# Performance work log

Hardware: AMD Instinct MI355X
Metric: run time of the kernel (lower is better)

## Reference

```python
import jax, jax.numpy as jnp
import numpy as np


def log_g(x):
    # Appendix B.3 of 'Were RNNs All We Needed?'
    return jnp.where(x >= 0, jnp.log(jax.nn.relu(x) + 0.5), -jax.nn.softplus(-x))


def parallel_scan_log(log_a, log_b):
    # h[0] = b[0]; h[i] = a[i]*h[i-1] + b[i], computed in log space along axis 1
    log_a_star = jnp.cumsum(log_a, axis=1)
    log_x0_plus_b_star = jax.lax.cumlogsumexp(log_b - log_a_star, axis=1)
    return jnp.exp(log_a_star + log_x0_plus_b_star)


def setup_inputs() -> dict:
    key = jax.random.key(0)
    B, T, D = 8, 4096, 1024
    k1, k2, k3, k4, k5 = jax.random.split(key, 5)
    scale = 1.0 / np.sqrt(D)
    return {
        "h_prev_layer": jax.random.normal(k1, (B, T, D), dtype=jnp.float32),
        "W_z": jax.random.uniform(k2, (D, D), jnp.float32, -scale, scale),
        "b_z": jax.random.uniform(k3, (D,), jnp.float32, -scale, scale),
        "W_h": jax.random.uniform(k4, (D, D), jnp.float32, -scale, scale),
        "b_h": jax.random.uniform(k5, (D,), jnp.float32, -scale, scale),
    }


def reference(h_prev_layer, W_z, b_z, W_h, b_h):
    k = jnp.einsum('btd,ed->bte', h_prev_layer, W_z) + b_z          # linear_z
    tilde_h = jnp.einsum('btd,ed->bte', h_prev_layer, W_h) + b_h    # linear_h
    log_z = -jax.nn.softplus(-k)
    log_one_minus_z = -jax.nn.softplus(k)
    log_tilde_h = log_g(tilde_h)
    return parallel_scan_log(log_one_minus_z, log_z + log_tilde_h)
```

## Files before the change

kernel.cpp:

```cpp
#include <hip/hip_runtime.h>
#include <hip/hip_fp16.h>

typedef float f32x4 __attribute__((ext_vector_type(4)));
typedef __bf16 bf16x8 __attribute__((ext_vector_type(8)));

#define BB_ 8
#define TT_ 4096
#define DD_ 1024
#define MM_ (BB_*TT_)
#define KK_ DD_

#define NCH 64
#define LCH (TT_/NCH)

static __device__ __forceinline__ unsigned short f2bf_rn(float f) {
  unsigned int u = __float_as_uint(f);
  u += 0x7FFFu + ((u >> 16) & 1u);
  return (unsigned short)(u >> 16);
}

__global__ void cvt_f32_bf16(const float4* __restrict__ src,
                             ushort4* __restrict__ dst, int n4) {
  int stride = gridDim.x * blockDim.x;
  for (int i = blockIdx.x * blockDim.x + threadIdx.x; i < n4; i += stride) {
    float4 v = src[i];
    ushort4 o;
    o.x = f2bf_rn(v.x); o.y = f2bf_rn(v.y);
    o.z = f2bf_rn(v.z); o.w = f2bf_rn(v.w);
    dst[i] = o;
  }
}

__device__ __forceinline__ void gload_lds16(const void* g, void* l) {
  __builtin_amdgcn_global_load_lds(
      (const __attribute__((address_space(1))) void*)g,
      (__attribute__((address_space(3))) void*)l, 16, 0, 0);
}

#define STA(q, nb_, kkh) gload_lds16(pXa + (q) * 65536 + (kkh), (nb_) + (q) * 8192 + wofs)
#define STB(q, nb_, kkh) gload_lds16(pWb + (q) * 65536 + (kkh), (nb_) + 32768 + (q) * 8192 + wofs)

#define PHASE(cb_, mh, kh, STAGEOPS, WAITOPS) do {                          \
    const char* Ab_ = (cb_);                                                \
    const char* Bb_ = (cb_) + 32768;                                        \
    const int sk_ = (kh) ? sk1 : sk0;                                       \
    bf16x8 af_[4];                                                          \
    _Pragma("unroll")                                                       \
    for (int ii = 0; ii < 4; ++ii)                                          \
      af_[ii] = *reinterpret_cast<const bf16x8*>(                           \
          Ab_ + rA7 + (mh) * 8192 + ii * 2048 + sk_);                       \
    if ((mh) == 0) {                                                        \
      _Pragma("unroll")                                                     \
      for (int j = 0; j < 4; ++j)                                           \
        bfv[j] = *reinterpret_cast<const bf16x8*>(                          \
            Bb_ + rB7 + j * 2048 + sk_);                                    \
    }                                                                       \
    STAGEOPS;                                                               \
    WAITOPS;                                                                \
    __builtin_amdgcn_s_barrier();                                           \
    asm volatile("s_waitcnt lgkmcnt(0)" ::: "memory");                      \
    __builtin_amdgcn_sched_barrier(0);                                      \
    __builtin_amdgcn_s_setprio(1);                                          \
    _Pragma("unroll")                                                       \
    for (int ii = 0; ii < 4; ++ii)                                          \
      _Pragma("unroll")                                                     \
      for (int j = 0; j < 4; ++j)                                           \
        acc[(mh) * 4 + ii][j] = __builtin_amdgcn_mfma_f32_16x16x32_bf16(    \
            af_[ii], bfv[j], acc[(mh) * 4 + ii][j], 0, 0, 0);               \
    __builtin_amdgcn_s_setprio(0);                                          \
    asm volatile("" ::: "memory");                                          \
    __builtin_amdgcn_s_barrier();                                           \
  } while (0)

__global__ __launch_bounds__(512, 2) void gemm_fused(
    const unsigned short* __restrict__ Xb,
    const unsigned short* __restrict__ Wb,
    const float* __restrict__ bz, const float* __restrict__ bh,
    __half* __restrict__ Zb, __half* __restrict__ Gb)
{
  extern __shared__ __align__(16) char smem[];
  const int tid  = threadIdx.x;
  const int wave = tid >> 6;
  const int lane = tid & 63;
  const int wm = wave >> 2, wn = wave & 3;
  const int fr = lane & 15, kg = lane >> 4, fx = fr & 7;

  int swz = (blockIdx.x & 7) * 128 + (blockIdx.x >> 3);
  const int m0 = (swz >> 3) * 256;
  const int e0 = (swz & 7) * 256;

  const int arow = tid >> 3;
  const int aslx = ((tid & 7) ^ (arow & 7)) * 8;
  const unsigned short* pXa = Xb + (size_t)(m0 + arow) * KK_ + aslx;
  const unsigned short* pWb = Wb + (size_t)(e0 + arow) * KK_ + aslx;
  const int wofs = wave * 1024;

  const int rA7 = (wm * 128 + fr) * 128;
  const int rB7 = (wn * 64 + fr) * 128;
  const int sk0 = (kg ^ fx) * 16;
  const int sk1 = sk0 ^ 64;

  f32x4 acc[8][4];
  #pragma unroll
  for (int i = 0; i < 8; i++)
    #pragma unroll
    for (int j = 0; j < 4; j++)
      acc[i][j] = (f32x4){0.f, 0.f, 0.f, 0.f};
  bf16x8 bfv[4];

  STA(0, smem, 0); STA(2, smem, 0); STB(0, smem, 0);
  STB(1, smem, 0); STB(2, smem, 0); STB(3, smem, 0);
  STA(1, smem, 0); STA(3, smem, 0);
  asm volatile("s_waitcnt vmcnt(2)" ::: "memory");
  __builtin_amdgcn_s_barrier();

  #pragma unroll 1
  for (int t = 0; t < 15; ++t) {
    char* cb = smem + ((t & 1) << 16);
    char* nb = smem + (((t + 1) & 1) << 16);
    const int kn = (t + 1) * 64;
    PHASE(cb, 0, 0, {STA(0, nb, kn); STA(2, nb, kn); STB(0, nb, kn);},
          asm volatile("s_waitcnt vmcnt(3)" ::: "memory"));
    PHASE(cb, 1, 0, {STB(1, nb, kn); STB(2, nb, kn); STB(3, nb, kn);}, );
    PHASE(cb, 0, 1, {STA(1, nb, kn); STA(3, nb, kn);}, );
    PHASE(cb, 1, 1, {},
          asm volatile("s_waitcnt vmcnt(2)" ::: "memory"));
  }
  {
    char* cb = smem + 65536;
    PHASE(cb, 0, 0, {}, asm volatile("s_waitcnt vmcnt(0)" ::: "memory"));
    PHASE(cb, 1, 0, {}, );
    PHASE(cb, 0, 1, {}, );
    PHASE(cb, 1, 1, {}, );
  }

  const bool isZ = (e0 < DD_);
  const float* bias = isZ ? bz : bh;
  __half* outp = isZ ? Zb : Gb;
  const int ec0 = (isZ ? e0 : (e0 - DD_)) + wn * 64;

  float bv[4];
  #pragma unroll
  for (int j = 0; j < 4; j++) bv[j] = bias[ec0 + j * 16 + fr];

  __half* ew = (__half*)(smem + wave * 9216);
  const int sub = lane & 7, rowr = lane >> 3;

  #pragma unroll
  for (int p = 0; p < 2; ++p) {
    #pragma unroll
    for (int ii = 0; ii < 4; ++ii) {
      #pragma unroll
      for (int j = 0; j < 4; ++j) {
        #pragma unroll
        for (int r = 0; r < 4; ++r) {
          float val = acc[p * 4 + ii][j][r] + bv[j];
          float res;
          if (isZ) {
            res = 1.0f / (1.0f + __expf(-val));
          } else {
            res = (val >= 0.0f) ? (val + 0.5f)
                                : (1.0f / (1.0f + __expf(-val)));
          }
          ew[(ii * 16 + kg * 4 + r) * 72 + j * 16 + fr] = __float2half(res);
        }
      }
    }
    #pragma unroll
    for (int q = 0; q < 8; ++q) {
      int rl = q * 8 + rowr;
      uint4 v = *reinterpret_cast<const uint4*>(&ew[rl * 72 + sub * 8]);
      size_t rg = (size_t)(m0 + wm * 128 + p * 64 + rl);
      *reinterpret_cast<uint4*>(&outp[rg * DD_ + ec0 + sub * 8]) = v;
    }
  }
}

__global__ __launch_bounds__(256) void scan_partial(
    const ushort4* __restrict__ Z, const ushort4* __restrict__ G,
    float4* __restrict__ P, float4* __restrict__ Q) {
  const int d4 = threadIdx.x;
  const int c  = blockIdx.x;
  const int b  = blockIdx.y;
  size_t base = ((size_t)b * TT_ + (size_t)c * LCH) * (DD_ / 4) + d4;
  float p0=1.f,p1=1.f,p2=1.f,p3=1.f, q0=0.f,q1=0.f,q2=0.f,q3=0.f;
  for (int t = 0; t < LCH; ++t) {
    ushort4 uz = Z[base + (size_t)t * (DD_ / 4)];
    ushort4 ug = G[base + (size_t)t * (DD_ / 4)];
    float z, g, a;
    z = __half2float(__ushort_as_half(uz.x)); g = __half2float(__ushort_as_half(ug.x));
    a = 1.f - z; p0 *= a; q0 = fmaf(a, q0, z * g);
    z = __half2float(__ushort_as_half(uz.y)); g = __half2float(__ushort_as_half(ug.y));
    a = 1.f - z; p1 *= a; q1 = fmaf(a, q1, z * g);
    z = __half2float(__ushort_as_half(uz.z)); g = __half2float(__ushort_as_half(ug.z));
    a = 1.f - z; p2 *= a; q2 = fmaf(a, q2, z * g);
    z = __half2float(__ushort_as_half(uz.w)); g = __half2float(__ushort_as_half(ug.w));
    a = 1.f - z; p3 *= a; q3 = fmaf(a, q3, z * g);
  }
  size_t o = ((size_t)b * NCH + c) * (DD_ / 4) + d4;
  P[o] = make_float4(p0, p1, p2, p3);
  Q[o] = make_float4(q0, q1, q2, q3);
}

__global__ __launch_bounds__(256) void scan_combine(
    const float4* __restrict__ P, const float4* __restrict__ Q,
    float4* __restrict__ H) {
  const int d4 = threadIdx.x;
  const int b  = blockIdx.x;
  float4 h = make_float4(0.f, 0.f, 0.f, 0.f);
  for (int c = 0; c < NCH; ++c) {
    size_t o = ((size_t)b * NCH + c) * (DD_ / 4) + d4;
    H[o] = h;
    float4 p = P[o], q = Q[o];
    h.x = fmaf(p.x, h.x, q.x);
    h.y = fmaf(p.y, h.y, q.y);
    h.z = fmaf(p.z, h.z, q.z);
    h.w = fmaf(p.w, h.w, q.w);
  }
}

__global__ __launch_bounds__(256) void scan_apply(
    const ushort4* __restrict__ Z, const ushort4* __restrict__ G,
    const float4* __restrict__ H, float4* __restrict__ out) {
  const int d4 = threadIdx.x;
  const int c  = blockIdx.x;
  const int b  = blockIdx.y;
  float4 h = H[((size_t)b * NCH + c) * (DD_ / 4) + d4];
  size_t base = ((size_t)b * TT_ + (size_t)c * LCH) * (DD_ / 4) + d4;
  for (int t = 0; t < LCH; ++t) {
    ushort4 uz = Z[base + (size_t)t * (DD_ / 4)];
    ushort4 ug = G[base + (size_t)t * (DD_ / 4)];
    float z, g, a;
    z = __half2float(__ushort_as_half(uz.x)); g = __half2float(__ushort_as_half(ug.x));
    a = 1.f - z; h.x = fmaf(a, h.x, z * g);
    z = __half2float(__ushort_as_half(uz.y)); g = __half2float(__ushort_as_half(ug.y));
    a = 1.f - z; h.y = fmaf(a, h.y, z * g);
    z = __half2float(__ushort_as_half(uz.z)); g = __half2float(__ushort_as_half(ug.z));
    a = 1.f - z; h.z = fmaf(a, h.z, z * g);
    z = __half2float(__ushort_as_half(uz.w)); g = __half2float(__ushort_as_half(ug.w));
    a = 1.f - z; h.w = fmaf(a, h.w, z * g);
    out[base + (size_t)t * (DD_ / 4)] = h;
  }
}

extern "C" void kernel_launch(void* const* d_in, const int* in_sizes, int n_in,
                              void* d_out, int out_size, void* d_ws, size_t ws_size,
                              hipStream_t stream) {
  const float* X  = (const float*)d_in[0];
  const float* Wz = (const float*)d_in[1];
  const float* bz = (const float*)d_in[2];
  const float* Wh = (const float*)d_in[3];
  const float* bh = (const float*)d_in[4];
  float* out = (float*)d_out;

  const size_t szXb = (size_t)MM_ * DD_ * 2;
  const size_t szWb = (size_t)2 * DD_ * DD_ * 2;
  const size_t szZ  = (size_t)MM_ * DD_ * 2;
  const size_t szPQ = (size_t)BB_ * NCH * DD_ * 4;

  char* ws = (char*)d_ws;
  unsigned short *Xb, *Wb;
  __half *Zb, *Gb;
  const size_t needA = szXb + szWb + 2 * szZ + 3 * szPQ;
  if (ws_size >= needA) {
    Xb = (unsigned short*)ws;              ws += szXb;
    Wb = (unsigned short*)ws;              ws += szWb;
  } else {
    Xb = (unsigned short*)d_out;
    Wb = (unsigned short*)((char*)d_out + szXb);
  }
  Zb = (__half*)ws;  ws += szZ;
  Gb = (__half*)ws;  ws += szZ;
  float* P = (float*)ws;  ws += szPQ;
  float* Q = (float*)ws;  ws += szPQ;
  float* H = (float*)ws;

  cvt_f32_bf16<<<2048, 256, 0, stream>>>((const float4*)X, (ushort4*)Xb,
                                         (int)((size_t)MM_ * DD_ / 4));
  cvt_f32_bf16<<<512, 256, 0, stream>>>((const float4*)Wz, (ushort4*)Wb,
                                        DD_ * DD_ / 4);
  cvt_f32_bf16<<<512, 256, 0, stream>>>((const float4*)Wh,
                                        (ushort4*)(Wb + (size_t)DD_ * DD_),
                                        DD_ * DD_ / 4);
  gemm_fused<<<(MM_ / 256) * ((2 * DD_) / 256), 512, 131072, stream>>>(
      Xb, Wb, bz, bh, Zb, Gb);

  scan_partial<<<dim3(NCH, BB_), 256, 0, stream>>>((const ushort4*)Zb, (const ushort4*)Gb,
                                                   (float4*)P, (float4*)Q);
  scan_combine<<<BB_, 256, 0, stream>>>((const float4*)P, (const float4*)Q, (float4*)H);
  scan_apply<<<dim3(NCH, BB_), 256, 0, stream>>>((const ushort4*)Zb, (const ushort4*)Gb,
                                                 (const float4*)H, (float4*)out);
}
```

Baseline: 280.1 us.

## Double-buffer LDS fragment registers to overlap ds_reads with MFMA in GEMM mainloop

Restructures the GEMM main loop so the LDS fragment reads for the next phase go into a second register set while the current phase's MFMAs execute. Partial lgkmcnt waits (8) replace full drains. All eight global-to-LDS stages for the next tile are now issued together, with a single vmcnt(0) wait before that buffer is consumed. This aims to hide LDS read latency behind matrix math, at the cost of more VGPRs (B fragments are reloaded every phase) and possible occupancy pressure under launch_bounds(512,2).

```diff
diff --git a/kernel.cpp b/kernel.cpp
--- a/kernel.cpp
+++ b/kernel.cpp
@@ -40,37 +40,37 @@
 #define STA(q, nb_, kkh) gload_lds16(pXa + (q) * 65536 + (kkh), (nb_) + (q) * 8192 + wofs)
 #define STB(q, nb_, kkh) gload_lds16(pWb + (q) * 65536 + (kkh), (nb_) + 32768 + (q) * 8192 + wofs)
 
-#define PHASE(cb_, mh, kh, STAGEOPS, WAITOPS) do {                          \
-    const char* Ab_ = (cb_);                                                \
-    const char* Bb_ = (cb_) + 32768;                                        \
-    const int sk_ = (kh) ? sk1 : sk0;                                       \
-    bf16x8 af_[4];                                                          \
+#define LOADF(DA, DB, base_, mh, kh) do {                                   \
+    const char* A__ = (base_);                                              \
+    const char* B__ = (base_) + 32768;                                      \
+    const int s__ = (kh) ? sk1 : sk0;                                       \
     _Pragma("unroll")                                                       \
     for (int ii = 0; ii < 4; ++ii)                                          \
-      af_[ii] = *reinterpret_cast<const bf16x8*>(                           \
-          Ab_ + rA7 + (mh) * 8192 + ii * 2048 + sk_);                       \
-    if ((mh) == 0) {                                                        \
-      _Pragma("unroll")                                                     \
-      for (int j = 0; j < 4; ++j)                                           \
-        bfv[j] = *reinterpret_cast<const bf16x8*>(                          \
-            Bb_ + rB7 + j * 2048 + sk_);                                    \
-    }                                                                       \
-    STAGEOPS;                                                               \
-    WAITOPS;                                                                \
-    __builtin_amdgcn_s_barrier();                                           \
-    asm volatile("s_waitcnt lgkmcnt(0)" ::: "memory");                      \
-    __builtin_amdgcn_sched_barrier(0);                                      \
+      DA[ii] = *reinterpret_cast<const bf16x8*>(                            \
+          A__ + rA7 + (mh) * 8192 + ii * 2048 + s__);                       \
+    _Pragma("unroll")                                                       \
+    for (int j = 0; j < 4; ++j)                                             \
+      DB[j] = *reinterpret_cast<const bf16x8*>(B__ + rB7 + j * 2048 + s__); \
+  } while (0)
+
+#define MFMAQ(SA, SB, mh) do {                                              \
     __builtin_amdgcn_s_setprio(1);                                          \
     _Pragma("unroll")                                                       \
     for (int ii = 0; ii < 4; ++ii)                                          \
       _Pragma("unroll")                                                     \
       for (int j = 0; j < 4; ++j)                                           \
         acc[(mh) * 4 + ii][j] = __builtin_amdgcn_mfma_f32_16x16x32_bf16(    \
-            af_[ii], bfv[j], acc[(mh) * 4 + ii][j], 0, 0, 0);               \
+            SA[ii], SB[j], acc[(mh) * 4 + ii][j], 0, 0, 0);                 \
     __builtin_amdgcn_s_setprio(0);                                          \
-    asm volatile("" ::: "memory");                                          \
-    __builtin_amdgcn_s_barrier();                                           \
   } while (0)
+
+#define BARSB() do { __builtin_amdgcn_s_barrier();                          \
+                     __builtin_amdgcn_sched_barrier(0); } while (0)
+#define LGKM8() do { asm volatile("s_waitcnt lgkmcnt(8)" ::: "memory");     \
+                     __builtin_amdgcn_sched_barrier(0); } while (0)
+#define LGKM0() do { asm volatile("s_waitcnt lgkmcnt(0)" ::: "memory");     \
+                     __builtin_amdgcn_sched_barrier(0); } while (0)
+#define VM0()   asm volatile("s_waitcnt vmcnt(0)" ::: "memory")
 
 __global__ __launch_bounds__(512, 2) void gemm_fused(
     const unsigned short* __restrict__ Xb,
@@ -106,32 +106,46 @@
     #pragma unroll
     for (int j = 0; j < 4; j++)
       acc[i][j] = (f32x4){0.f, 0.f, 0.f, 0.f};
-  bf16x8 bfv[4];
-
-  STA(0, smem, 0); STA(2, smem, 0); STB(0, smem, 0);
-  STB(1, smem, 0); STB(2, smem, 0); STB(3, smem, 0);
-  STA(1, smem, 0); STA(3, smem, 0);
-  asm volatile("s_waitcnt vmcnt(2)" ::: "memory");
+  bf16x8 afA[4], bvA[4], afB[4], bvB[4];
+
+  STA(0, smem, 0); STA(1, smem, 0); STA(2, smem, 0); STA(3, smem, 0);
+  STB(0, smem, 0); STB(1, smem, 0); STB(2, smem, 0); STB(3, smem, 0);
+  VM0();
   __builtin_amdgcn_s_barrier();
+  LOADF(afA, bvA, smem, 0, 0);
 
   #pragma unroll 1
   for (int t = 0; t < 15; ++t) {
     char* cb = smem + ((t & 1) << 16);
     char* nb = smem + (((t + 1) & 1) << 16);
     const int kn = (t + 1) * 64;
-    PHASE(cb, 0, 0, {STA(0, nb, kn); STA(2, nb, kn); STB(0, nb, kn);},
-          asm volatile("s_waitcnt vmcnt(3)" ::: "memory"));
-    PHASE(cb, 1, 0, {STB(1, nb, kn); STB(2, nb, kn); STB(3, nb, kn);}, );
-    PHASE(cb, 0, 1, {STA(1, nb, kn); STA(3, nb, kn);}, );
-    PHASE(cb, 1, 1, {},
-          asm volatile("s_waitcnt vmcnt(2)" ::: "memory"));
+    BARSB();
+    LOADF(afB, bvB, cb, 1, 0);
+    STA(0, nb, kn); STA(1, nb, kn); STA(2, nb, kn); STA(3, nb, kn);
+    STB(0, nb, kn); STB(1, nb, kn); STB(2, nb, kn); STB(3, nb, kn);
+    LGKM8();
+    MFMAQ(afA, bvA, 0);
+    BARSB();
+    LOADF(afA, bvA, cb, 0, 1);
+    LGKM8();
+    MFMAQ(afB, bvB, 1);
+    BARSB();
+    LOADF(afB, bvB, cb, 1, 1);
+    VM0();
+    LGKM8();
+    MFMAQ(afA, bvA, 0);
+    BARSB();
+    LOADF(afA, bvA, nb, 0, 0);
+    LGKM8();
+    MFMAQ(afB, bvB, 1);
   }
   {
     char* cb = smem + 65536;
-    PHASE(cb, 0, 0, {}, asm volatile("s_waitcnt vmcnt(0)" ::: "memory"));
-    PHASE(cb, 1, 0, {}, );
-    PHASE(cb, 0, 1, {}, );
-    PHASE(cb, 1, 1, {}, );
+    BARSB(); LOADF(afB, bvB, cb, 1, 0); LGKM8(); MFMAQ(afA, bvA, 0);
+    BARSB(); LOADF(afA, bvA, cb, 0, 1); LGKM8(); MFMAQ(afB, bvB, 1);
+    BARSB(); LOADF(afB, bvB, cb, 1, 1); LGKM8(); MFMAQ(afA, bvA, 0);
+    BARSB(); LGKM0();                   MFMAQ(afB, bvB, 1);
+    __builtin_amdgcn_s_barrier();
   }
 
   const bool isZ = (e0 < DD_);
```

New measurement: 300.2 us. 1.07x slower.

## Deepen GEMM LDS pipeline to four stages with K=32 tiles; widen scan_combine grid

Applied to the files above, without the earlier changes.

The GEMM main loop moves from two 64-wide K buffers of 64KB each to four 32-wide K buffers of 32KB each, with loads issued three stages ahead and a new XOR swizzle suited to 64-byte rows. The goal is to hide more global-load latency behind MFMA work within the same LDS budget. The cost is more barriers per unit of K and a longer drain sequence. Separately, scan_combine is spread over 32 blocks of scalar threads instead of 8 blocks using float4, which gives the serial chunk combine more parallelism.

```diff
diff --git a/kernel.cpp b/kernel.cpp
--- a/kernel.cpp
+++ b/kernel.cpp
@@ -37,23 +37,20 @@
       (__attribute__((address_space(3))) void*)l, 16, 0, 0);
 }
 
-#define STA(q, nb_, kkh) gload_lds16(pXa + (q) * 65536 + (kkh), (nb_) + (q) * 8192 + wofs)
-#define STB(q, nb_, kkh) gload_lds16(pWb + (q) * 65536 + (kkh), (nb_) + 32768 + (q) * 8192 + wofs)
-
-#define PHASE(cb_, mh, kh, STAGEOPS, WAITOPS) do {                          \
-    const char* Ab_ = (cb_);                                                \
-    const char* Bb_ = (cb_) + 32768;                                        \
-    const int sk_ = (kh) ? sk1 : sk0;                                       \
+#define STA2(q, buf_, kkh) gload_lds16(pXa + (size_t)(q) * 131072 + (kkh), (buf_) + (q) * 8192 + wofs)
+#define STB2(q, buf_, kkh) gload_lds16(pWb + (size_t)(q) * 131072 + (kkh), (buf_) + 16384 + (q) * 8192 + wofs)
+
+#define PH(buf_, mh, STAGEOPS, WAITOPS) do {                                \
+    const char* Ab_ = (const char*)(buf_);                                  \
     bf16x8 af_[4];                                                          \
     _Pragma("unroll")                                                       \
     for (int ii = 0; ii < 4; ++ii)                                          \
       af_[ii] = *reinterpret_cast<const bf16x8*>(                           \
-          Ab_ + rA7 + (mh) * 8192 + ii * 2048 + sk_);                       \
+          Ab_ + rAb + (mh) * 4096 + ii * 1024);                             \
     if ((mh) == 0) {                                                        \
       _Pragma("unroll")                                                     \
       for (int j = 0; j < 4; ++j)                                           \
-        bfv[j] = *reinterpret_cast<const bf16x8*>(                          \
-            Bb_ + rB7 + j * 2048 + sk_);                                    \
+        bfv[j] = *reinterpret_cast<const bf16x8*>(Ab_ + rBb + j * 1024);    \
     }                                                                       \
     STAGEOPS;                                                               \
     WAITOPS;                                                                \
@@ -72,6 +69,8 @@
     __builtin_amdgcn_s_barrier();                                           \
   } while (0)
 
+#define VMW(n) asm volatile("s_waitcnt vmcnt(" #n ")" ::: "memory")
+
 __global__ __launch_bounds__(512, 2) void gemm_fused(
     const unsigned short* __restrict__ Xb,
     const unsigned short* __restrict__ Wb,
@@ -83,22 +82,21 @@
   const int wave = tid >> 6;
   const int lane = tid & 63;
   const int wm = wave >> 2, wn = wave & 3;
-  const int fr = lane & 15, kg = lane >> 4, fx = fr & 7;
+  const int fr = lane & 15, kg = lane >> 4;
 
   int swz = (blockIdx.x & 7) * 128 + (blockIdx.x >> 3);
   const int m0 = (swz >> 3) * 256;
   const int e0 = (swz & 7) * 256;
 
-  const int arow = tid >> 3;
-  const int aslx = ((tid & 7) ^ (arow & 7)) * 8;
-  const unsigned short* pXa = Xb + (size_t)(m0 + arow) * KK_ + aslx;
-  const unsigned short* pWb = Wb + (size_t)(e0 + arow) * KK_ + aslx;
+  const int arow2 = tid >> 2;
+  const int ac = ((tid & 3) ^ (arow2 & 3)) * 8;
+  const unsigned short* pXa = Xb + (size_t)(m0 + arow2) * KK_ + ac;
+  const unsigned short* pWb = Wb + (size_t)(e0 + arow2) * KK_ + ac;
   const int wofs = wave * 1024;
 
-  const int rA7 = (wm * 128 + fr) * 128;
-  const int rB7 = (wn * 64 + fr) * 128;
-  const int sk0 = (kg ^ fx) * 16;
-  const int sk1 = sk0 ^ 64;
+  const int cksw = ((kg ^ (fr & 3)) << 4);
+  const int rAb = (wm * 128 + fr) * 64 + cksw;
+  const int rBb = 16384 + (wn * 64 + fr) * 64 + cksw;
 
   f32x4 acc[8][4];
   #pragma unroll
@@ -108,30 +106,33 @@
       acc[i][j] = (f32x4){0.f, 0.f, 0.f, 0.f};
   bf16x8 bfv[4];
 
-  STA(0, smem, 0); STA(2, smem, 0); STB(0, smem, 0);
-  STB(1, smem, 0); STB(2, smem, 0); STB(3, smem, 0);
-  STA(1, smem, 0); STA(3, smem, 0);
-  asm volatile("s_waitcnt vmcnt(2)" ::: "memory");
+  STA2(0, smem, 0);           STA2(1, smem, 0);
+  STB2(0, smem, 0);           STB2(1, smem, 0);
+  STA2(0, smem + 32768, 32);  STA2(1, smem + 32768, 32);
+  STB2(0, smem + 32768, 32);  STB2(1, smem + 32768, 32);
+  STA2(0, smem + 65536, 64);  STA2(1, smem + 65536, 64);
+  STB2(0, smem + 65536, 64);  STB2(1, smem + 65536, 64);
+  VMW(8);
   __builtin_amdgcn_s_barrier();
 
   #pragma unroll 1
-  for (int t = 0; t < 15; ++t) {
-    char* cb = smem + ((t & 1) << 16);
-    char* nb = smem + (((t + 1) & 1) << 16);
-    const int kn = (t + 1) * 64;
-    PHASE(cb, 0, 0, {STA(0, nb, kn); STA(2, nb, kn); STB(0, nb, kn);},
-          asm volatile("s_waitcnt vmcnt(3)" ::: "memory"));
-    PHASE(cb, 1, 0, {STB(1, nb, kn); STB(2, nb, kn); STB(3, nb, kn);}, );
-    PHASE(cb, 0, 1, {STA(1, nb, kn); STA(3, nb, kn);}, );
-    PHASE(cb, 1, 1, {},
-          asm volatile("s_waitcnt vmcnt(2)" ::: "memory"));
+  for (int t = 0; t < 29; ++t) {
+    const char* cb = smem + ((t & 3) << 15);
+    char* nb = smem + (((t + 3) & 3) << 15);
+    const int kn = (t + 3) * 32;
+    PH(cb, 0, {STA2(0, nb, kn); STA2(1, nb, kn);}, );
+    PH(cb, 1, {STB2(0, nb, kn); STB2(1, nb, kn);}, VMW(8));
   }
   {
-    char* cb = smem + 65536;
-    PHASE(cb, 0, 0, {}, asm volatile("s_waitcnt vmcnt(0)" ::: "memory"));
-    PHASE(cb, 1, 0, {}, );
-    PHASE(cb, 0, 1, {}, );
-    PHASE(cb, 1, 1, {}, );
+    const char* b1 = smem + 32768;
+    const char* b2 = smem + 65536;
+    const char* b3 = smem + 98304;
+    PH(b1, 0, {}, );
+    PH(b1, 1, {}, VMW(4));
+    PH(b2, 0, {}, );
+    PH(b2, 1, {}, VMW(0));
+    PH(b3, 0, {}, );
+    PH(b3, 1, {}, );
   }
 
   const bool isZ = (e0 < DD_);
@@ -203,19 +204,15 @@
 }
 
 __global__ __launch_bounds__(256) void scan_combine(
-    const float4* __restrict__ P, const float4* __restrict__ Q,
-    float4* __restrict__ H) {
-  const int d4 = threadIdx.x;
-  const int b  = blockIdx.x;
-  float4 h = make_float4(0.f, 0.f, 0.f, 0.f);
+    const float* __restrict__ P, const float* __restrict__ Q,
+    float* __restrict__ H) {
+  const int d = blockIdx.x * 256 + threadIdx.x;
+  const int b = blockIdx.y;
+  float h = 0.f;
   for (int c = 0; c < NCH; ++c) {
-    size_t o = ((size_t)b * NCH + c) * (DD_ / 4) + d4;
+    size_t o = ((size_t)b * NCH + c) * DD_ + d;
     H[o] = h;
-    float4 p = P[o], q = Q[o];
-    h.x = fmaf(p.x, h.x, q.x);
-    h.y = fmaf(p.y, h.y, q.y);
-    h.z = fmaf(p.z, h.z, q.z);
-    h.w = fmaf(p.w, h.w, q.w);
+    h = fmaf(P[o], h, Q[o]);
   }
 }
 
@@ -287,7 +284,7 @@
 
   scan_partial<<<dim3(NCH, BB_), 256, 0, stream>>>((const ushort4*)Zb, (const ushort4*)Gb,
                                                    (float4*)P, (float4*)Q);
-  scan_combine<<<BB_, 256, 0, stream>>>((const float4*)P, (const float4*)Q, (float4*)H);
+  scan_combine<<<dim3(4, BB_), 256, 0, stream>>>(P, Q, H);
   scan_apply<<<dim3(NCH, BB_), 256, 0, stream>>>((const ushort4*)Zb, (const ushort4*)Gb,
                                                  (const float4*)H, (float4*)out);
 }
```

New measurement: 289.3 us. 3.3% more time.

## Fuse chunk-partial scan into GEMM epilogue via interleaved Z/H weight layout

Applied to the files above, without the earlier changes.

Reorders the concatenated weight rows so each 256-column GEMM tile holds 128 matching z and h columns, letting the epilogue stage both gates in shared memory and compute the per-chunk scan partials (P,Q) directly. This removes the separate scan_partial kernel and its full re-read of Z and G from global memory. scan_combine is also widened to more blocks with scalar indexing. The epilogue now adds a block-wide sync and a serial 64-step loop per thread, which lengthens the GEMM tail.

```diff
diff --git a/kernel.cpp b/kernel.cpp
--- a/kernel.cpp
+++ b/kernel.cpp
@@ -29,6 +29,22 @@
     o.z = f2bf_rn(v.z); o.w = f2bf_rn(v.w);
     dst[i] = o;
   }
+}
+
+__global__ void cvt_w(const float4* __restrict__ Wz4,
+                      const float4* __restrict__ Wh4,
+                      ushort4* __restrict__ Wcat) {
+  int flat = blockIdx.x * 256 + threadIdx.x;
+  int mtx = flat >> 18;
+  int j = flat & 262143;
+  float4 v = (mtx ? Wh4 : Wz4)[j];
+  int D = j >> 8;
+  int kq = j & 255;
+  int row = ((D >> 7) << 8) + (mtx << 7) + (D & 127);
+  ushort4 o;
+  o.x = f2bf_rn(v.x); o.y = f2bf_rn(v.y);
+  o.z = f2bf_rn(v.z); o.w = f2bf_rn(v.w);
+  Wcat[(size_t)row * 256 + kq] = o;
 }
 
 __device__ __forceinline__ void gload_lds16(const void* g, void* l) {
@@ -76,18 +92,20 @@
     const unsigned short* __restrict__ Xb,
     const unsigned short* __restrict__ Wb,
     const float* __restrict__ bz, const float* __restrict__ bh,
-    __half* __restrict__ Zb, __half* __restrict__ Gb)
+    __half* __restrict__ Zb, __half* __restrict__ Gb,
+    float* __restrict__ Pp, float* __restrict__ Qq)
 {
   extern __shared__ __align__(16) char smem[];
   const int tid  = threadIdx.x;
   const int wave = tid >> 6;
   const int lane = tid & 63;
   const int wm = wave >> 2, wn = wave & 3;
-  const int fr = lane & 15, kg = lane >> 4, fx = fr & 7;
+  const int fr = lane & 15, kg = lane >> 4;
 
   int swz = (blockIdx.x & 7) * 128 + (blockIdx.x >> 3);
   const int m0 = (swz >> 3) * 256;
   const int e0 = (swz & 7) * 256;
+  const int dg = swz & 7;
 
   const int arow = tid >> 3;
   const int aslx = ((tid & 7) ^ (arow & 7)) * 8;
@@ -97,6 +115,7 @@
 
   const int rA7 = (wm * 128 + fr) * 128;
   const int rB7 = (wn * 64 + fr) * 128;
+  const int fx = fr & 7;
   const int sk0 = (kg ^ fx) * 16;
   const int sk1 = sk0 ^ 64;
 
@@ -134,88 +153,99 @@
     PHASE(cb, 1, 1, {}, );
   }
 
-  const bool isZ = (e0 < DD_);
+  __half* sc = (__half*)smem;
+  const bool isZ = (wn < 2);
+  const int dloc0 = (wn & 1) * 64;
+  const int zg = isZ ? 0 : 1;
   const float* bias = isZ ? bz : bh;
-  __half* outp = isZ ? Zb : Gb;
-  const int ec0 = (isZ ? e0 : (e0 - DD_)) + wn * 64;
-
-  float bv[4];
+  float bvv[4];
   #pragma unroll
-  for (int j = 0; j < 4; j++) bv[j] = bias[ec0 + j * 16 + fr];
-
-  __half* ew = (__half*)(smem + wave * 9216);
-  const int sub = lane & 7, rowr = lane >> 3;
+  for (int j = 0; j < 4; ++j) bvv[j] = bias[dg * 128 + dloc0 + j * 16 + fr];
 
   #pragma unroll
-  for (int p = 0; p < 2; ++p) {
+  for (int a = 0; a < 8; ++a) {
+    const int tl = wm * 128 + (a >> 2) * 64 + (a & 3) * 16 + kg * 4;
     #pragma unroll
-    for (int ii = 0; ii < 4; ++ii) {
+    for (int j = 0; j < 4; ++j) {
+      const int d = dloc0 + j * 16 + fr;
       #pragma unroll
-      for (int j = 0; j < 4; ++j) {
-        #pragma unroll
-        for (int r = 0; r < 4; ++r) {
-          float val = acc[p * 4 + ii][j][r] + bv[j];
-          float res;
-          if (isZ) {
-            res = 1.0f / (1.0f + __expf(-val));
-          } else {
-            res = (val >= 0.0f) ? (val + 0.5f)
-                                : (1.0f / (1.0f + __expf(-val)));
-          }
-          ew[(ii * 16 + kg * 4 + r) * 72 + j * 16 + fr] = __float2half(res);
+      for (int r = 0; r < 4; ++r) {
+        float val = acc[a][j][r] + bvv[j];
+        float res;
+        if (isZ) {
+          res = 1.0f / (1.0f + __expf(-val));
+        } else {
+          res = (val >= 0.0f) ? (val + 0.5f)
+                              : (1.0f / (1.0f + __expf(-val)));
         }
+        const int t = tl + r;
+        sc[t * 256 + ((d >> 2) ^ (t & 15)) * 8 + (d & 3) * 2 + zg] =
+            __float2half(res);
       }
     }
+  }
+  __syncthreads();
+
+  {
+    const int dl = tid & 127, cgl = tid >> 7;
+    const int dq = dl >> 2, dlo = (dl & 3) * 2;
+    float pp = 1.f, qq = 0.f;
+    #pragma unroll 4
+    for (int i = 0; i < 64; ++i) {
+      const int t = cgl * 64 + i;
+      unsigned int zw = *reinterpret_cast<const unsigned int*>(
+          &sc[t * 256 + ((dq ^ (t & 15)) * 8) + dlo]);
+      float z = __half2float(__ushort_as_half((unsigned short)(zw & 0xffff)));
+      float g = __half2float(__ushort_as_half((unsigned short)(zw >> 16)));
+      float aa = 1.f - z;
+      pp *= aa;
+      qq = fmaf(aa, qq, z * g);
+    }
+    const int b = m0 >> 12;
+    const int cg = ((m0 & 4095) >> 6) + cgl;
+    size_t po = ((size_t)b * NCH + cg) * DD_ + dg * 128 + dl;
+    Pp[po] = pp;
+    Qq[po] = qq;
+  }
+
+  {
+    const int row = tid >> 1, hd = tid & 1;
+    const size_t rg = (size_t)m0 + row;
+    __half* zdst = Zb + rg * DD_ + dg * 128 + hd * 64;
+    __half* gdst = Gb + rg * DD_ + dg * 128 + hd * 64;
+    const int t = row;
     #pragma unroll
-    for (int q = 0; q < 8; ++q) {
-      int rl = q * 8 + rowr;
-      uint4 v = *reinterpret_cast<const uint4*>(&ew[rl * 72 + sub * 8]);
-      size_t rg = (size_t)(m0 + wm * 128 + p * 64 + rl);
-      *reinterpret_cast<uint4*>(&outp[rg * DD_ + ec0 + sub * 8]) = v;
+    for (int k = 0; k < 8; ++k) {
+      const int dq0 = hd * 16 + k * 2;
+      uint4 i0 = *reinterpret_cast<const uint4*>(
+          &sc[t * 256 + ((dq0 ^ (t & 15)) * 8)]);
+      uint4 i1 = *reinterpret_cast<const uint4*>(
+          &sc[t * 256 + (((dq0 + 1) ^ (t & 15)) * 8)]);
+      uint4 zv, gv;
+      zv.x = (i0.x & 0xffffu) | (i0.y << 16);
+      zv.y = (i0.z & 0xffffu) | (i0.w << 16);
+      zv.z = (i1.x & 0xffffu) | (i1.y << 16);
+      zv.w = (i1.z & 0xffffu) | (i1.w << 16);
+      gv.x = (i0.x >> 16) | (i0.y & 0xffff0000u);
+      gv.y = (i0.z >> 16) | (i0.w & 0xffff0000u);
+      gv.z = (i1.x >> 16) | (i1.y & 0xffff0000u);
+      gv.w = (i1.z >> 16) | (i1.w & 0xffff0000u);
+      *reinterpret_cast<uint4*>(zdst + k * 8) = zv;
+      *reinterpret_cast<uint4*>(gdst + k * 8) = gv;
     }
   }
 }
 
-__global__ __launch_bounds__(256) void scan_partial(
-    const ushort4* __restrict__ Z, const ushort4* __restrict__ G,
-    float4* __restrict__ P, float4* __restrict__ Q) {
-  const int d4 = threadIdx.x;
-  const int c  = blockIdx.x;
-  const int b  = blockIdx.y;
-  size_t base = ((size_t)b * TT_ + (size_t)c * LCH) * (DD_ / 4) + d4;
-  float p0=1.f,p1=1.f,p2=1.f,p3=1.f, q0=0.f,q1=0.f,q2=0.f,q3=0.f;
-  for (int t = 0; t < LCH; ++t) {
-    ushort4 uz = Z[base + (size_t)t * (DD_ / 4)];
-    ushort4 ug = G[base + (size_t)t * (DD_ / 4)];
-    float z, g, a;
-    z = __half2float(__ushort_as_half(uz.x)); g = __half2float(__ushort_as_half(ug.x));
-    a = 1.f - z; p0 *= a; q0 = fmaf(a, q0, z * g);
-    z = __half2float(__ushort_as_half(uz.y)); g = __half2float(__ushort_as_half(ug.y));
-    a = 1.f - z; p1 *= a; q1 = fmaf(a, q1, z * g);
-    z = __half2float(__ushort_as_half(uz.z)); g = __half2float(__ushort_as_half(ug.z));
-    a = 1.f - z; p2 *= a; q2 = fmaf(a, q2, z * g);
-    z = __half2float(__ushort_as_half(uz.w)); g = __half2float(__ushort_as_half(ug.w));
-    a = 1.f - z; p3 *= a; q3 = fmaf(a, q3, z * g);
-  }
-  size_t o = ((size_t)b * NCH + c) * (DD_ / 4) + d4;
-  P[o] = make_float4(p0, p1, p2, p3);
-  Q[o] = make_float4(q0, q1, q2, q3);
-}
-
 __global__ __launch_bounds__(256) void scan_combine(
-    const float4* __restrict__ P, const float4* __restrict__ Q,
-    float4* __restrict__ H) {
-  const int d4 = threadIdx.x;
-  const int b  = blockIdx.x;
-  float4 h = make_float4(0.f, 0.f, 0.f, 0.f);
+    const float* __restrict__ P, const float* __restrict__ Q,
+    float* __restrict__ H) {
+  const int d = blockIdx.x * 256 + threadIdx.x;
+  const int b = blockIdx.y;
+  float h = 0.f;
   for (int c = 0; c < NCH; ++c) {
-    size_t o = ((size_t)b * NCH + c) * (DD_ / 4) + d4;
+    size_t o = ((size_t)b * NCH + c) * DD_ + d;
     H[o] = h;
-    float4 p = P[o], q = Q[o];
-    h.x = fmaf(p.x, h.x, q.x);
-    h.y = fmaf(p.y, h.y, q.y);
-    h.z = fmaf(p.z, h.z, q.z);
-    h.w = fmaf(p.w, h.w, q.w);
+    h = fmaf(P[o], h, Q[o]);
   }
 }
 
@@ -277,17 +307,12 @@
 
   cvt_f32_bf16<<<2048, 256, 0, stream>>>((const float4*)X, (ushort4*)Xb,
                                          (int)((size_t)MM_ * DD_ / 4));
-  cvt_f32_bf16<<<512, 256, 0, stream>>>((const float4*)Wz, (ushort4*)Wb,
-                                        DD_ * DD_ / 4);
-  cvt_f32_bf16<<<512, 256, 0, stream>>>((const float4*)Wh,
-                                        (ushort4*)(Wb + (size_t)DD_ * DD_),
-                                        DD_ * DD_ / 4);
+  cvt_w<<<2048, 256, 0, stream>>>((const float4*)Wz, (const float4*)Wh,
+                                  (ushort4*)Wb);
   gemm_fused<<<(MM_ / 256) * ((2 * DD_) / 256), 512, 131072, stream>>>(
-      Xb, Wb, bz, bh, Zb, Gb);
-
-  scan_partial<<<dim3(NCH, BB_), 256, 0, stream>>>((const ushort4*)Zb, (const ushort4*)Gb,
-                                                   (float4*)P, (float4*)Q);
-  scan_combine<<<BB_, 256, 0, stream>>>((const float4*)P, (const float4*)Q, (float4*)H);
+      Xb, Wb, bz, bh, Zb, Gb, P, Q);
+
+  scan_combine<<<dim3(4, BB_), 256, 0, stream>>>(P, Q, H);
   scan_apply<<<dim3(NCH, BB_), 256, 0, stream>>>((const ushort4*)Zb, (const ushort4*)Gb,
                                                  (const float4*)H, (float4*)out);
 }
```

Measured after the change: 318.5 us. +13.7%, slower.
